# Kernel tuning notes

Measured on AMD Instinct MI355X. Metric: run time of the kernel, lower is better.

## Reference

```python
import jax, jax.numpy as jnp
import numpy as np

N, M, D, O = 16384, 4096, 256, 256

def setup_inputs() -> dict:
    key = jax.random.key(0)
    k1, k2, k3, k4, k5, k6, k7 = jax.random.split(key, 7)
    H_fine = jax.random.normal(k1, (N, D), dtype=jnp.float32)
    H_coarse = jax.random.normal(k2, (M, D), dtype=jnp.float32)
    inter_channel_adj = jax.random.randint(k3, (N, M), 0, 2).astype(jnp.float32)
    # attention = nn.Linear(2D, 1): weight vector [2D], bias scalar
    wa = jax.random.normal(k4, (2 * D,), dtype=jnp.float32) * (1.0 / np.sqrt(2 * D))
    ba = jax.random.normal(k5, (1,), dtype=jnp.float32) * 0.01
    # transform = nn.Linear(D, O), xavier_uniform weight
    lim = np.sqrt(6.0 / (D + O)).astype(np.float32)
    Wt = jax.random.uniform(k6, (O, D), minval=-lim, maxval=lim, dtype=jnp.float32)
    bt = jax.random.normal(k7, (O,), dtype=jnp.float32) * 0.01
    return {"H_fine": H_fine, "H_coarse": H_coarse,
            "inter_channel_adj": inter_channel_adj,
            "wa": wa, "ba": ba, "Wt": Wt, "bt": bt}

def reference(H_fine, H_coarse, inter_channel_adj, wa, ba, Wt, bt):
    d = H_fine.shape[-1]
    # additive attention: score_ij = [hf_i ; hc_j] . wa + b
    # = hf_i . wa[:d] + hc_j . wa[d:] + b  (avoids [N,M,2D] concat)
    sf = H_fine @ wa[:d]            # [N]
    sc = H_coarse @ wa[d:]          # [M]
    scores = sf[:, None] + sc[None, :] + ba[0]        # [N, M]
    masked = scores * inter_channel_adj               # [N, M]
    weights = jax.nn.softmax(masked, axis=-1)         # [N, M]
    attn_out = weights @ H_coarse                     # [N, D]
    attn_out = attn_out + H_fine                      # add_self=True
    out = attn_out @ Wt.T + bt                        # [N, O]
    return jax.nn.relu(out)
```

## Files before the change

### kernel.cpp

```cpp
#include <hip/hip_runtime.h>
#include <hip/hip_bf16.h>
#include <stdint.h>

#define N_ 16384
#define M_ 4096
#define D_ 256
#define O_ 256

#define WS_T    0
#define WS_U    (64*1024)
#define WS_R    (80*1024)
#define WS_WTP  (96*1024)
#define WS_BP   (256*1024)

typedef float  f32x4  __attribute__((ext_vector_type(4)));
typedef short  short8 __attribute__((ext_vector_type(8)));

__device__ __forceinline__ unsigned short f2bf(float f) {
  uint32_t u = __float_as_uint(f);
  u += 0x7FFFu + ((u >> 16) & 1u);
  return (unsigned short)(u >> 16);
}
__device__ __forceinline__ uint32_t pack2bf(float a, float b) {
  return (uint32_t)f2bf(a) | ((uint32_t)f2bf(b) << 16);
}

__device__ __forceinline__ void gload_lds16(const void* g, void* l) {
  __builtin_amdgcn_global_load_lds(
      (const __attribute__((address_space(1))) void*)g,
      (__attribute__((address_space(3))) void*)l, 16, 0, 0);
}

__global__ __launch_bounds__(256) void rowdot_exp_kernel(
    const float* __restrict__ X, const float* __restrict__ w,
    const float* __restrict__ bias, float* __restrict__ outv) {
  int wv = threadIdx.x >> 6, lane = threadIdx.x & 63;
  int row = blockIdx.x * 4 + wv;
  const float4* x4 = (const float4*)(X + (size_t)row * D_);
  const float4* w4 = (const float4*)w;
  float4 xa = x4[lane], wa4 = w4[lane];
  float s = xa.x * wa4.x + xa.y * wa4.y + xa.z * wa4.z + xa.w * wa4.w;
#pragma unroll
  for (int off = 32; off > 0; off >>= 1) s += __shfl_xor(s, off);
  if (lane == 0) outv[row] = expf(s + (bias ? bias[0] : 0.0f));
}

__global__ __launch_bounds__(256) void hc_pack_kernel(
    const float* __restrict__ Hc, unsigned short* __restrict__ BP,
    float* __restrict__ R) {
  __shared__ float tile[64][65];
  __shared__ float red[4][64];
  int bk = blockIdx.x >> 2;
  int bc = blockIdx.x & 3;
  int k0 = bk * 64, col0 = bc * 64;
  int t = threadIdx.x;
  int lane = t & 63, wv = t >> 6;
  int m = lane & 15, q = lane >> 4;
  float colsum = 0.0f;
#pragma unroll
  for (int i = 0; i < 16; ++i) {
    int e = t + 256 * i;
    int kk = e >> 6, cc = e & 63;
    float v = Hc[(size_t)(k0 + kk) * D_ + col0 + cc];
    tile[kk][cc] = v;
    colsum += v;
  }
  red[wv][t & 63] = colsum;
  __syncthreads();
  if (t < 64)
    atomicAdd(&R[col0 + t], red[0][t] + red[1][t] + red[2][t] + red[3][t]);
#pragma unroll
  for (int t8 = 0; t8 < 2; ++t8) {
    int tile_id = t8 * 4 + wv;
    int sub = tile_id >> 2, g = tile_id & 3;
    int kgg = bk * 2 + sub;
    int cgg = bc * 4 + g;
    short8 v8;
#pragma unroll
    for (int j = 0; j < 8; ++j)
      v8[j] = (short)f2bf(tile[sub * 32 + q * 8 + j][g * 16 + m]);
    *(short8*)(BP + ((size_t)(kgg * 16 + cgg) * 64 + lane) * 8) = v8;
  }
}

__global__ __launch_bounds__(256) void wt_pack_kernel(
    const float* __restrict__ Wt, unsigned short* __restrict__ WtP) {
  int t = blockIdx.x * 256 + threadIdx.x;
  int lane = t & 63, cg = (t >> 6) & 15, kg = t >> 10;
  int m = lane & 15, q = lane >> 4;
  const float* src = Wt + (size_t)(cg * 16 + m) * D_ + kg * 32 + q * 8;
  float4 w0 = *(const float4*)src, w1 = *(const float4*)(src + 4);
  short8 v8;
  v8[0] = (short)f2bf(w0.x); v8[1] = (short)f2bf(w0.y);
  v8[2] = (short)f2bf(w0.z); v8[3] = (short)f2bf(w0.w);
  v8[4] = (short)f2bf(w1.x); v8[5] = (short)f2bf(w1.y);
  v8[6] = (short)f2bf(w1.z); v8[7] = (short)f2bf(w1.w);
  *(short8*)(WtP + (size_t)t * 8) = v8;
}

__global__ __launch_bounds__(512, 4) void main_fused_kernel(
    const float* __restrict__ adj, const unsigned short* __restrict__ BP,
    const float* __restrict__ tv, const float* __restrict__ uv,
    const float* __restrict__ Rv, const float* __restrict__ Hf,
    const unsigned short* __restrict__ WtP, const float* __restrict__ bt,
    float* __restrict__ out) {
  union SM {
    struct {
      unsigned short B[2][16][512];
      unsigned int   A[2][2][256];
    } st;
    unsigned short attn[32][264];
  };
  __shared__ SM sm;
  __shared__ float Lrow[32];

  int tid = threadIdx.x;
  int w = tid >> 6, lane = tid & 63;
  int rtile = w & 1, cq = w >> 1;
  int q = lane >> 4, m = lane & 15;
  int i0 = blockIdx.x * 32;

  int srow = tid >> 4;
  int kin  = (tid & 15) * 2;
  int rts  = srow >> 4;
  int sdw  = (((kin >> 3) * 16 + (srow & 15)) << 2) + ((kin & 7) >> 1);
  const float* adjp = adj + (size_t)(i0 + srow) * M_ + kin;
  const float* up   = uv + kin;
  float t_reg = tv[i0 + srow];

  f32x4 acc[4];
#pragma unroll
  for (int n = 0; n < 4; ++n) acc[n] = (f32x4){0.f, 0.f, 0.f, 0.f};
  float rs = 0.0f;

#pragma unroll
  for (int c = 0; c < 2; ++c) {
    int cg = w * 2 + c;
    gload_lds16(BP + ((size_t)cg * 64 + lane) * 8, &sm.st.B[0][cg][0]);
  }
  {
    float2 a0 = *(const float2*)adjp;
    float2 uu = *(const float2*)up;
    float p0 = fmaf(a0.x, t_reg * uu.x, -a0.x);
    float p1 = fmaf(a0.y, t_reg * uu.y, -a0.y);
    rs += p0 + p1;
    sm.st.A[0][rts][sdw] = pack2bf(p0, p1);
  }
  float2 aA = *(const float2*)(adjp + 32);
  float2 aB = *(const float2*)(adjp + 64);
  __syncthreads();

  for (int kc = 0; kc < 128; ++kc) {
    int buf = kc & 1, nbuf = buf ^ 1;
    if (kc < 127) {
#pragma unroll
      for (int c = 0; c < 2; ++c) {
        int cg = w * 2 + c;
        gload_lds16(BP + ((size_t)((kc + 1) * 16 + cg) * 64 + lane) * 8,
                    &sm.st.B[nbuf][cg][0]);
      }
    }
    int k3 = (kc + 3 < 128) ? (kc + 3) * 32 : 0;
    float2 aC = *(const float2*)(adjp + k3);

    short8 af = *(const short8*)((const unsigned short*)&sm.st.A[buf][rtile][0] +
                                 (size_t)lane * 8);
#pragma unroll
    for (int n = 0; n < 4; ++n) {
      short8 bf = *(const short8*)&sm.st.B[buf][cq * 4 + n][lane * 8];
      acc[n] = __builtin_amdgcn_mfma_f32_16x16x32_bf16(af, bf, acc[n], 0, 0, 0);
    }

    if (kc < 127) {
      float2 uu = *(const float2*)(up + (kc + 1) * 32);
      float p0 = fmaf(aA.x, t_reg * uu.x, -aA.x);
      float p1 = fmaf(aA.y, t_reg * uu.y, -aA.y);
      rs += p0 + p1;
      sm.st.A[nbuf][rts][sdw] = pack2bf(p0, p1);
    }
    aA = aB; aB = aC;
    __syncthreads();
  }

  rs += __shfl_xor(rs, 1);
  rs += __shfl_xor(rs, 2);
  rs += __shfl_xor(rs, 4);
  rs += __shfl_xor(rs, 8);
  if ((lane & 15) == 0) Lrow[w * 4 + (lane >> 4)] = rs;
  __syncthreads();

  float invL[4];
#pragma unroll
  for (int r = 0; r < 4; ++r)
    invL[r] = 1.0f / (Lrow[rtile * 16 + q * 4 + r] + (float)M_);

#pragma unroll
  for (int n = 0; n < 4; ++n) {
    int col = cq * 64 + n * 16 + m;
    float Rc = Rv[col];
#pragma unroll
    for (int r = 0; r < 4; ++r) {
      int rloc = rtile * 16 + q * 4 + r;
      size_t row = (size_t)i0 + rloc;
      float v = (acc[n][r] + Rc) * invL[r] + Hf[row * D_ + col];
      sm.attn[rloc][col] = f2bf(v);
    }
  }
  __syncthreads();

  f32x4 facc[4];
#pragma unroll
  for (int n = 0; n < 4; ++n) facc[n] = (f32x4){0.f, 0.f, 0.f, 0.f};
  const unsigned short* wwave = WtP + (size_t)(cq * 4) * 512 + (size_t)lane * 8;
#pragma unroll
  for (int kf = 0; kf < 8; ++kf) {
    short8 af = *(const short8*)&sm.attn[rtile * 16 + m][kf * 32 + q * 8];
#pragma unroll
    for (int n = 0; n < 4; ++n) {
      short8 bf = *(const short8*)(wwave + ((size_t)kf * 16 + n) * 512);
      facc[n] = __builtin_amdgcn_mfma_f32_16x16x32_bf16(af, bf, facc[n], 0, 0, 0);
    }
  }
#pragma unroll
  for (int n = 0; n < 4; ++n) {
    int col = cq * 64 + n * 16 + m;
    float b = bt[col];
#pragma unroll
    for (int r = 0; r < 4; ++r) {
      size_t row = (size_t)i0 + rtile * 16 + q * 4 + r;
      out[row * O_ + col] = fmaxf(facc[n][r] + b, 0.0f);
    }
  }
}

extern "C" void kernel_launch(void* const* d_in, const int* in_sizes, int n_in,
                              void* d_out, int out_size, void* d_ws, size_t ws_size,
                              hipStream_t stream) {
  const float* Hf  = (const float*)d_in[0];
  const float* Hc  = (const float*)d_in[1];
  const float* adj = (const float*)d_in[2];
  const float* wa  = (const float*)d_in[3];
  const float* ba  = (const float*)d_in[4];
  const float* Wt  = (const float*)d_in[5];
  const float* bt  = (const float*)d_in[6];
  float* out = (float*)d_out;

  char* ws = (char*)d_ws;
  float* tv = (float*)(ws + WS_T);
  float* uv = (float*)(ws + WS_U);
  float* Rv = (float*)(ws + WS_R);
  unsigned short* WtP = (unsigned short*)(ws + WS_WTP);
  unsigned short* BP  = (unsigned short*)(ws + WS_BP);

  hipMemsetAsync(Rv, 0, D_ * sizeof(float), stream);

  rowdot_exp_kernel<<<N_ / 4, 256, 0, stream>>>(Hf, wa, ba, tv);
  rowdot_exp_kernel<<<M_ / 4, 256, 0, stream>>>(Hc, wa + D_, nullptr, uv);
  hc_pack_kernel<<<256, 256, 0, stream>>>(Hc, BP, Rv);
  wt_pack_kernel<<<32, 256, 0, stream>>>(Wt, WtP);

  main_fused_kernel<<<N_ / 32, 512, 0, stream>>>(adj, BP, tv, uv, Rv, Hf, WtP, bt, out);
}
```

Before: 537.2 us.

## Split attention matmul over K halves with atomic reduction and separate epilogue

Replaces the single fused kernel with a split-K kernel: each of two blocks per 32-row tile handles half of the coarse dimension. The kernel reads adj and packed H_coarse straight into registers instead of staging through LDS with per-step barriers, and accumulates partial results and row sums into global buffers with atomics. A separate epilogue kernel then normalizes, adds H_fine and runs the output projection. The aim is more parallelism and removal of barrier stalls in the bandwidth-bound adj stream, at the cost of an extra 16 MB memset, atomic traffic and one more launch.

```diff
diff --git a/kernel.cpp b/kernel.cpp
--- a/kernel.cpp
+++ b/kernel.cpp
@@ -7,11 +7,13 @@
 #define D_ 256
 #define O_ 256
 
-#define WS_T    0
-#define WS_U    (64*1024)
-#define WS_R    (80*1024)
-#define WS_WTP  (96*1024)
-#define WS_BP   (256*1024)
+#define WS_T     0
+#define WS_U     65536
+#define WS_R     81920
+#define WS_LSUM  98304
+#define WS_WTP   163840
+#define WS_BP    294912
+#define WS_C     4194304
 
 typedef float  f32x4  __attribute__((ext_vector_type(4)));
 typedef short  short8 __attribute__((ext_vector_type(8)));
@@ -20,15 +22,6 @@
   uint32_t u = __float_as_uint(f);
   u += 0x7FFFu + ((u >> 16) & 1u);
   return (unsigned short)(u >> 16);
-}
-__device__ __forceinline__ uint32_t pack2bf(float a, float b) {
-  return (uint32_t)f2bf(a) | ((uint32_t)f2bf(b) << 16);
-}
-
-__device__ __forceinline__ void gload_lds16(const void* g, void* l) {
-  __builtin_amdgcn_global_load_lds(
-      (const __attribute__((address_space(1))) void*)g,
-      (__attribute__((address_space(3))) void*)l, 16, 0, 0);
 }
 
 __global__ __launch_bounds__(256) void rowdot_exp_kernel(
@@ -98,132 +91,161 @@
   *(short8*)(WtP + (size_t)t * 8) = v8;
 }
 
-__global__ __launch_bounds__(512, 4) void main_fused_kernel(
+__global__ __launch_bounds__(256, 4) void main_split_kernel(
     const float* __restrict__ adj, const unsigned short* __restrict__ BP,
     const float* __restrict__ tv, const float* __restrict__ uv,
+    float* __restrict__ Cbuf, float* __restrict__ Lsum) {
+  __shared__ float u_lds[2048];
+  int tid = threadIdx.x;
+  int w = tid >> 6, lane = tid & 63;
+  int q = lane >> 4, m = lane & 15;
+  int kh = blockIdx.x & 1, rb = blockIdx.x >> 1;
+  int i0 = rb * 32;
+  int c0 = w * 64;
+
+  for (int i = tid; i < 2048; i += 256) u_lds[i] = uv[kh * 2048 + i];
+
+  float t0 = tv[i0 + m], t1 = tv[i0 + 16 + m];
+  const float* ar0 = adj + (size_t)(i0 + m) * M_ + kh * 2048 + q * 8;
+  const float* ar1 = ar0 + (size_t)16 * M_;
+  const unsigned short* bb = BP + (size_t)(kh * 64 * 16 + w * 4) * 512 + (size_t)lane * 8;
+
+  f32x4 acc[2][4];
+#pragma unroll
+  for (int r = 0; r < 2; ++r)
+#pragma unroll
+    for (int n = 0; n < 4; ++n) acc[r][n] = (f32x4){0.f, 0.f, 0.f, 0.f};
+  float rs0 = 0.0f, rs1 = 0.0f;
+
+  __syncthreads();
+
+  float4 aX00 = *(const float4*)ar0, aX01 = *(const float4*)(ar0 + 4);
+  float4 aX10 = *(const float4*)ar1, aX11 = *(const float4*)(ar1 + 4);
+  short8 bX[4], bY[4];
+#pragma unroll
+  for (int n = 0; n < 4; ++n) bX[n] = *(const short8*)(bb + n * 512);
+  float4 aY00, aY01, aY10, aY11;
+
+#define XF(A0, A1, TR, U0, U1, RS, AF)                                  \
+  {                                                                     \
+    float ax[8] = {A0.x, A0.y, A0.z, A0.w, A1.x, A1.y, A1.z, A1.w};     \
+    float ux[8] = {U0.x, U0.y, U0.z, U0.w, U1.x, U1.y, U1.z, U1.w};     \
+    _Pragma("unroll") for (int j = 0; j < 8; ++j) {                     \
+      float p = fmaf(ax[j], TR * ux[j], -ax[j]);                        \
+      RS += p;                                                          \
+      AF[j] = (short)f2bf(p);                                           \
+    }                                                                   \
+  }
+
+  for (int kk = 0; kk < 64; kk += 2) {
+    {
+      const float* p0 = ar0 + (kk + 1) * 32;
+      const float* p1 = ar1 + (kk + 1) * 32;
+      aY00 = *(const float4*)p0; aY01 = *(const float4*)(p0 + 4);
+      aY10 = *(const float4*)p1; aY11 = *(const float4*)(p1 + 4);
+      const unsigned short* bp = bb + (size_t)(kk + 1) * 8192;
+#pragma unroll
+      for (int n = 0; n < 4; ++n) bY[n] = *(const short8*)(bp + n * 512);
+    }
+    {
+      float4 u0 = *(const float4*)&u_lds[kk * 32 + q * 8];
+      float4 u1 = *(const float4*)&u_lds[kk * 32 + q * 8 + 4];
+      short8 af0, af1;
+      XF(aX00, aX01, t0, u0, u1, rs0, af0);
+      XF(aX10, aX11, t1, u0, u1, rs1, af1);
+#pragma unroll
+      for (int n = 0; n < 4; ++n) {
+        acc[0][n] = __builtin_amdgcn_mfma_f32_16x16x32_bf16(af0, bX[n], acc[0][n], 0, 0, 0);
+        acc[1][n] = __builtin_amdgcn_mfma_f32_16x16x32_bf16(af1, bX[n], acc[1][n], 0, 0, 0);
+      }
+    }
+    {
+      int k2 = (kk + 2) & 63;
+      const float* p0 = ar0 + k2 * 32;
+      const float* p1 = ar1 + k2 * 32;
+      aX00 = *(const float4*)p0; aX01 = *(const float4*)(p0 + 4);
+      aX10 = *(const float4*)p1; aX11 = *(const float4*)(p1 + 4);
+      const unsigned short* bp = bb + (size_t)k2 * 8192;
+#pragma unroll
+      for (int n = 0; n < 4; ++n) bX[n] = *(const short8*)(bp + n * 512);
+    }
+    {
+      float4 u0 = *(const float4*)&u_lds[(kk + 1) * 32 + q * 8];
+      float4 u1 = *(const float4*)&u_lds[(kk + 1) * 32 + q * 8 + 4];
+      short8 af0, af1;
+      XF(aY00, aY01, t0, u0, u1, rs0, af0);
+      XF(aY10, aY11, t1, u0, u1, rs1, af1);
+#pragma unroll
+      for (int n = 0; n < 4; ++n) {
+        acc[0][n] = __builtin_amdgcn_mfma_f32_16x16x32_bf16(af0, bY[n], acc[0][n], 0, 0, 0);
+        acc[1][n] = __builtin_amdgcn_mfma_f32_16x16x32_bf16(af1, bY[n], acc[1][n], 0, 0, 0);
+      }
+    }
+  }
+#undef XF
+
+  rs0 += __shfl_xor(rs0, 16); rs0 += __shfl_xor(rs0, 32);
+  rs1 += __shfl_xor(rs1, 16); rs1 += __shfl_xor(rs1, 32);
+  if (w == 0 && lane < 16) {
+    atomicAdd(&Lsum[i0 + m], rs0);
+    atomicAdd(&Lsum[i0 + 16 + m], rs1);
+  }
+
+#pragma unroll
+  for (int r = 0; r < 2; ++r)
+#pragma unroll
+    for (int n = 0; n < 4; ++n) {
+      int col = c0 + n * 16 + m;
+#pragma unroll
+      for (int j = 0; j < 4; ++j) {
+        int row = i0 + r * 16 + q * 4 + j;
+        atomicAdd(&Cbuf[(size_t)row * D_ + col], acc[r][n][j]);
+      }
+    }
+}
+
+__global__ __launch_bounds__(256, 4) void epilogue_kernel(
+    const float* __restrict__ Cbuf, const float* __restrict__ Lsum,
     const float* __restrict__ Rv, const float* __restrict__ Hf,
     const unsigned short* __restrict__ WtP, const float* __restrict__ bt,
     float* __restrict__ out) {
-  union SM {
-    struct {
-      unsigned short B[2][16][512];
-      unsigned int   A[2][2][256];
-    } st;
-    unsigned short attn[32][264];
-  };
-  __shared__ SM sm;
-  __shared__ float Lrow[32];
-
+  __shared__ alignas(16) unsigned short attn[32][264];
   int tid = threadIdx.x;
   int w = tid >> 6, lane = tid & 63;
-  int rtile = w & 1, cq = w >> 1;
+  int rtile = w & 1, chalf = w >> 1;
   int q = lane >> 4, m = lane & 15;
   int i0 = blockIdx.x * 32;
 
-  int srow = tid >> 4;
-  int kin  = (tid & 15) * 2;
-  int rts  = srow >> 4;
-  int sdw  = (((kin >> 3) * 16 + (srow & 15)) << 2) + ((kin & 7) >> 1);
-  const float* adjp = adj + (size_t)(i0 + srow) * M_ + kin;
-  const float* up   = uv + kin;
-  float t_reg = tv[i0 + srow];
-
-  f32x4 acc[4];
-#pragma unroll
-  for (int n = 0; n < 4; ++n) acc[n] = (f32x4){0.f, 0.f, 0.f, 0.f};
-  float rs = 0.0f;
-
-#pragma unroll
-  for (int c = 0; c < 2; ++c) {
-    int cg = w * 2 + c;
-    gload_lds16(BP + ((size_t)cg * 64 + lane) * 8, &sm.st.B[0][cg][0]);
-  }
-  {
-    float2 a0 = *(const float2*)adjp;
-    float2 uu = *(const float2*)up;
-    float p0 = fmaf(a0.x, t_reg * uu.x, -a0.x);
-    float p1 = fmaf(a0.y, t_reg * uu.y, -a0.y);
-    rs += p0 + p1;
-    sm.st.A[0][rts][sdw] = pack2bf(p0, p1);
-  }
-  float2 aA = *(const float2*)(adjp + 32);
-  float2 aB = *(const float2*)(adjp + 64);
+  float4 rv = *(const float4*)(Rv + lane * 4);
+#pragma unroll
+  for (int rr = 0; rr < 8; ++rr) {
+    int r = w * 8 + rr;
+    float invL = 1.0f / (Lsum[i0 + r] + (float)M_);
+    float4 cv = *(const float4*)(Cbuf + (size_t)(i0 + r) * D_ + lane * 4);
+    float4 hv = *(const float4*)(Hf + (size_t)(i0 + r) * D_ + lane * 4);
+    attn[r][lane * 4 + 0] = f2bf(fmaf(cv.x + rv.x, invL, hv.x));
+    attn[r][lane * 4 + 1] = f2bf(fmaf(cv.y + rv.y, invL, hv.y));
+    attn[r][lane * 4 + 2] = f2bf(fmaf(cv.z + rv.z, invL, hv.z));
+    attn[r][lane * 4 + 3] = f2bf(fmaf(cv.w + rv.w, invL, hv.w));
+  }
   __syncthreads();
 
-  for (int kc = 0; kc < 128; ++kc) {
-    int buf = kc & 1, nbuf = buf ^ 1;
-    if (kc < 127) {
-#pragma unroll
-      for (int c = 0; c < 2; ++c) {
-        int cg = w * 2 + c;
-        gload_lds16(BP + ((size_t)((kc + 1) * 16 + cg) * 64 + lane) * 8,
-                    &sm.st.B[nbuf][cg][0]);
-      }
-    }
-    int k3 = (kc + 3 < 128) ? (kc + 3) * 32 : 0;
-    float2 aC = *(const float2*)(adjp + k3);
-
-    short8 af = *(const short8*)((const unsigned short*)&sm.st.A[buf][rtile][0] +
-                                 (size_t)lane * 8);
-#pragma unroll
-    for (int n = 0; n < 4; ++n) {
-      short8 bf = *(const short8*)&sm.st.B[buf][cq * 4 + n][lane * 8];
-      acc[n] = __builtin_amdgcn_mfma_f32_16x16x32_bf16(af, bf, acc[n], 0, 0, 0);
-    }
-
-    if (kc < 127) {
-      float2 uu = *(const float2*)(up + (kc + 1) * 32);
-      float p0 = fmaf(aA.x, t_reg * uu.x, -aA.x);
-      float p1 = fmaf(aA.y, t_reg * uu.y, -aA.y);
-      rs += p0 + p1;
-      sm.st.A[nbuf][rts][sdw] = pack2bf(p0, p1);
-    }
-    aA = aB; aB = aC;
-    __syncthreads();
-  }
-
-  rs += __shfl_xor(rs, 1);
-  rs += __shfl_xor(rs, 2);
-  rs += __shfl_xor(rs, 4);
-  rs += __shfl_xor(rs, 8);
-  if ((lane & 15) == 0) Lrow[w * 4 + (lane >> 4)] = rs;
-  __syncthreads();
-
-  float invL[4];
-#pragma unroll
-  for (int r = 0; r < 4; ++r)
-    invL[r] = 1.0f / (Lrow[rtile * 16 + q * 4 + r] + (float)M_);
-
-#pragma unroll
-  for (int n = 0; n < 4; ++n) {
-    int col = cq * 64 + n * 16 + m;
-    float Rc = Rv[col];
-#pragma unroll
-    for (int r = 0; r < 4; ++r) {
-      int rloc = rtile * 16 + q * 4 + r;
-      size_t row = (size_t)i0 + rloc;
-      float v = (acc[n][r] + Rc) * invL[r] + Hf[row * D_ + col];
-      sm.attn[rloc][col] = f2bf(v);
-    }
-  }
-  __syncthreads();
-
-  f32x4 facc[4];
-#pragma unroll
-  for (int n = 0; n < 4; ++n) facc[n] = (f32x4){0.f, 0.f, 0.f, 0.f};
-  const unsigned short* wwave = WtP + (size_t)(cq * 4) * 512 + (size_t)lane * 8;
+  f32x4 facc[8];
+#pragma unroll
+  for (int n = 0; n < 8; ++n) facc[n] = (f32x4){0.f, 0.f, 0.f, 0.f};
+  const unsigned short* wwave = WtP + (size_t)chalf * 4096 + (size_t)lane * 8;
 #pragma unroll
   for (int kf = 0; kf < 8; ++kf) {
-    short8 af = *(const short8*)&sm.attn[rtile * 16 + m][kf * 32 + q * 8];
-#pragma unroll
-    for (int n = 0; n < 4; ++n) {
+    short8 af = *(const short8*)&attn[rtile * 16 + m][kf * 32 + q * 8];
+#pragma unroll
+    for (int n = 0; n < 8; ++n) {
       short8 bf = *(const short8*)(wwave + ((size_t)kf * 16 + n) * 512);
       facc[n] = __builtin_amdgcn_mfma_f32_16x16x32_bf16(af, bf, facc[n], 0, 0, 0);
     }
   }
 #pragma unroll
-  for (int n = 0; n < 4; ++n) {
-    int col = cq * 64 + n * 16 + m;
+  for (int n = 0; n < 8; ++n) {
+    int col = chalf * 128 + n * 16 + m;
     float b = bt[col];
 #pragma unroll
     for (int r = 0; r < 4; ++r) {
@@ -246,18 +268,23 @@
   float* out = (float*)d_out;
 
   char* ws = (char*)d_ws;
-  float* tv = (float*)(ws + WS_T);
-  float* uv = (float*)(ws + WS_U);
-  float* Rv = (float*)(ws + WS_R);
+  float* tv   = (float*)(ws + WS_T);
+  float* uv   = (float*)(ws + WS_U);
+  float* Rv   = (float*)(ws + WS_R);
+  float* Lsum = (float*)(ws + WS_LSUM);
   unsigned short* WtP = (unsigned short*)(ws + WS_WTP);
   unsigned short* BP  = (unsigned short*)(ws + WS_BP);
+  float* Cbuf = (float*)(ws + WS_C);
 
   hipMemsetAsync(Rv, 0, D_ * sizeof(float), stream);
+  hipMemsetAsync(Lsum, 0, N_ * sizeof(float), stream);
+  hipMemsetAsync(Cbuf, 0, (size_t)N_ * D_ * sizeof(float), stream);
 
   rowdot_exp_kernel<<<N_ / 4, 256, 0, stream>>>(Hf, wa, ba, tv);
   rowdot_exp_kernel<<<M_ / 4, 256, 0, stream>>>(Hc, wa + D_, nullptr, uv);
   hc_pack_kernel<<<256, 256, 0, stream>>>(Hc, BP, Rv);
   wt_pack_kernel<<<32, 256, 0, stream>>>(Wt, WtP);
 
-  main_fused_kernel<<<N_ / 32, 512, 0, stream>>>(adj, BP, tv, uv, Rv, Hf, WtP, bt, out);
-}
+  main_split_kernel<<<N_ / 32 * 2, 256, 0, stream>>>(adj, BP, tv, uv, Cbuf, Lsum);
+  epilogue_kernel<<<N_ / 32, 256, 0, stream>>>(Cbuf, Lsum, Rv, Hf, WtP, bt, out);
+}
```

Result: slower. 612.7 us (+14.1%).

## Split K across waves in main kernel and reduce partial accumulators via LDS atomics

Applied to the files above, without the earlier changes.

The main kernel is restructured so each of the 8 waves handles a disjoint 512-column K slice of the adjacency for all 32 rows and all 256 output columns. B fragments are read straight from global/L2 instead of being staged through LDS with barriers, and u is cached in LDS. Partial results are combined with LDS atomicAdds before the epilogue. This removes the per-step __syncthreads and LDS staging of the old pipelined loop. In exchange it needs 128 accumulator registers per lane, drops occupancy to 2 blocks per CU, and adds many LDS atomics. The workspace offset for BP also moves.

```diff
diff --git a/kernel.cpp b/kernel.cpp
--- a/kernel.cpp
+++ b/kernel.cpp
@@ -8,10 +8,10 @@
 #define O_ 256
 
 #define WS_T    0
-#define WS_U    (64*1024)
-#define WS_R    (80*1024)
-#define WS_WTP  (96*1024)
-#define WS_BP   (256*1024)
+#define WS_U    65536
+#define WS_R    81920
+#define WS_WTP  98304
+#define WS_BP   229376
 
 typedef float  f32x4  __attribute__((ext_vector_type(4)));
 typedef short  short8 __attribute__((ext_vector_type(8)));
@@ -21,14 +21,11 @@
   u += 0x7FFFu + ((u >> 16) & 1u);
   return (unsigned short)(u >> 16);
 }
-__device__ __forceinline__ uint32_t pack2bf(float a, float b) {
-  return (uint32_t)f2bf(a) | ((uint32_t)f2bf(b) << 16);
-}
-
-__device__ __forceinline__ void gload_lds16(const void* g, void* l) {
-  __builtin_amdgcn_global_load_lds(
-      (const __attribute__((address_space(1))) void*)g,
-      (__attribute__((address_space(3))) void*)l, 16, 0, 0);
+__device__ __forceinline__ uint32_t cvtpk(float a, float b) {
+  __hip_bfloat162 h = __float22bfloat162_rn(float2{a, b});
+  uint32_t u;
+  __builtin_memcpy(&u, &h, 4);
+  return u;
 }
 
 __global__ __launch_bounds__(256) void rowdot_exp_kernel(
@@ -98,132 +95,150 @@
   *(short8*)(WtP + (size_t)t * 8) = v8;
 }
 
-__global__ __launch_bounds__(512, 4) void main_fused_kernel(
+__device__ __forceinline__ short8 transform8(float4 A0, float4 A1, float t,
+                                             float4 u0, float4 u1, float& rs) {
+  float p0 = fmaf(A0.x, t * u0.x, -A0.x);
+  float p1 = fmaf(A0.y, t * u0.y, -A0.y);
+  float p2 = fmaf(A0.z, t * u0.z, -A0.z);
+  float p3 = fmaf(A0.w, t * u0.w, -A0.w);
+  float p4 = fmaf(A1.x, t * u1.x, -A1.x);
+  float p5 = fmaf(A1.y, t * u1.y, -A1.y);
+  float p6 = fmaf(A1.z, t * u1.z, -A1.z);
+  float p7 = fmaf(A1.w, t * u1.w, -A1.w);
+  rs += ((p0 + p1) + (p2 + p3)) + ((p4 + p5) + (p6 + p7));
+  union { short8 s; uint32_t u[4]; } r;
+  r.u[0] = cvtpk(p0, p1);
+  r.u[1] = cvtpk(p2, p3);
+  r.u[2] = cvtpk(p4, p5);
+  r.u[3] = cvtpk(p6, p7);
+  return r.s;
+}
+
+__global__ __launch_bounds__(512, 2) void mega_kernel(
     const float* __restrict__ adj, const unsigned short* __restrict__ BP,
     const float* __restrict__ tv, const float* __restrict__ uv,
     const float* __restrict__ Rv, const float* __restrict__ Hf,
     const unsigned short* __restrict__ WtP, const float* __restrict__ bt,
     float* __restrict__ out) {
-  union SM {
-    struct {
-      unsigned short B[2][16][512];
-      unsigned int   A[2][2][256];
-    } st;
-    unsigned short attn[32][264];
-  };
-  __shared__ SM sm;
+  __shared__ float u_lds[M_];
+  __shared__ float part[32][260];
+  __shared__ float redd[8][32];
   __shared__ float Lrow[32];
+  __shared__ alignas(16) unsigned short attn[32][264];
 
   int tid = threadIdx.x;
   int w = tid >> 6, lane = tid & 63;
-  int rtile = w & 1, cq = w >> 1;
   int q = lane >> 4, m = lane & 15;
   int i0 = blockIdx.x * 32;
 
-  int srow = tid >> 4;
-  int kin  = (tid & 15) * 2;
-  int rts  = srow >> 4;
-  int sdw  = (((kin >> 3) * 16 + (srow & 15)) << 2) + ((kin & 7) >> 1);
-  const float* adjp = adj + (size_t)(i0 + srow) * M_ + kin;
-  const float* up   = uv + kin;
-  float t_reg = tv[i0 + srow];
-
-  f32x4 acc[4];
-#pragma unroll
-  for (int n = 0; n < 4; ++n) acc[n] = (f32x4){0.f, 0.f, 0.f, 0.f};
-  float rs = 0.0f;
-
-#pragma unroll
-  for (int c = 0; c < 2; ++c) {
-    int cg = w * 2 + c;
-    gload_lds16(BP + ((size_t)cg * 64 + lane) * 8, &sm.st.B[0][cg][0]);
-  }
+  for (int i = tid; i < M_; i += 512) u_lds[i] = uv[i];
   {
-    float2 a0 = *(const float2*)adjp;
-    float2 uu = *(const float2*)up;
-    float p0 = fmaf(a0.x, t_reg * uu.x, -a0.x);
-    float p1 = fmaf(a0.y, t_reg * uu.y, -a0.y);
-    rs += p0 + p1;
-    sm.st.A[0][rts][sdw] = pack2bf(p0, p1);
-  }
-  float2 aA = *(const float2*)(adjp + 32);
-  float2 aB = *(const float2*)(adjp + 64);
-  __syncthreads();
-
-  for (int kc = 0; kc < 128; ++kc) {
-    int buf = kc & 1, nbuf = buf ^ 1;
-    if (kc < 127) {
-#pragma unroll
-      for (int c = 0; c < 2; ++c) {
-        int cg = w * 2 + c;
-        gload_lds16(BP + ((size_t)((kc + 1) * 16 + cg) * 64 + lane) * 8,
-                    &sm.st.B[nbuf][cg][0]);
-      }
-    }
-    int k3 = (kc + 3 < 128) ? (kc + 3) * 32 : 0;
-    float2 aC = *(const float2*)(adjp + k3);
-
-    short8 af = *(const short8*)((const unsigned short*)&sm.st.A[buf][rtile][0] +
-                                 (size_t)lane * 8);
+    float* pz = &part[0][0];
+    for (int i = tid; i < 32 * 260; i += 512) pz[i] = 0.0f;
+  }
+
+  float t0 = tv[i0 + m], t1 = tv[i0 + 16 + m];
+  const float* a0 = adj + (size_t)(i0 + m) * M_ + w * 512 + q * 8;
+  const float* a1 = a0 + (size_t)16 * M_;
+
+  f32x4 acc[2][16];
+#pragma unroll
+  for (int s = 0; s < 2; ++s)
+#pragma unroll
+    for (int n = 0; n < 16; ++n) acc[s][n] = (f32x4){0.f, 0.f, 0.f, 0.f};
+  float rs0 = 0.0f, rs1 = 0.0f;
+
+  __syncthreads();
+
+  float4 pa0 = *(const float4*)(a0);
+  float4 pa1 = *(const float4*)(a0 + 4);
+  float4 pb0 = *(const float4*)(a1);
+  float4 pb1 = *(const float4*)(a1 + 4);
+
+  for (int i = 0; i < 16; ++i) {
+    int inx = (i + 1 < 16) ? i + 1 : 0;
+    float4 na0 = *(const float4*)(a0 + inx * 32);
+    float4 na1 = *(const float4*)(a0 + inx * 32 + 4);
+    float4 nb0 = *(const float4*)(a1 + inx * 32);
+    float4 nb1 = *(const float4*)(a1 + inx * 32 + 4);
+
+    int kg = w * 16 + i;
+    float4 u0 = *(const float4*)&u_lds[kg * 32 + q * 8];
+    float4 u1 = *(const float4*)&u_lds[kg * 32 + q * 8 + 4];
+    short8 af0 = transform8(pa0, pa1, t0, u0, u1, rs0);
+    short8 af1 = transform8(pb0, pb1, t1, u0, u1, rs1);
+
+    const unsigned short* bk = BP + (size_t)(kg * 16) * 512 + (size_t)lane * 8;
+    short8 bcur = *(const short8*)(bk);
+#pragma unroll
+    for (int n = 0; n < 16; ++n) {
+      short8 bnext = bcur;
+      if (n < 15) bnext = *(const short8*)(bk + (size_t)(n + 1) * 512);
+      acc[0][n] = __builtin_amdgcn_mfma_f32_16x16x32_bf16(af0, bcur, acc[0][n], 0, 0, 0);
+      acc[1][n] = __builtin_amdgcn_mfma_f32_16x16x32_bf16(af1, bcur, acc[1][n], 0, 0, 0);
+      bcur = bnext;
+    }
+    pa0 = na0; pa1 = na1; pb0 = nb0; pb1 = nb1;
+  }
+
+  rs0 += __shfl_xor(rs0, 16); rs0 += __shfl_xor(rs0, 32);
+  rs1 += __shfl_xor(rs1, 16); rs1 += __shfl_xor(rs1, 32);
+  if (lane < 16) { redd[w][m] = rs0; redd[w][16 + m] = rs1; }
+
+#pragma unroll
+  for (int s = 0; s < 2; ++s)
+#pragma unroll
+    for (int n = 0; n < 16; ++n) {
+      int col = n * 16 + m;
+#pragma unroll
+      for (int r = 0; r < 4; ++r)
+        atomicAdd(&part[s * 16 + q * 4 + r][col], acc[s][n][r]);
+    }
+  __syncthreads();
+
+  if (tid < 32) {
+    float S = 0.0f;
+#pragma unroll
+    for (int ww = 0; ww < 8; ++ww) S += redd[ww][tid];
+    Lrow[tid] = S;
+  }
+  __syncthreads();
+
+#pragma unroll
+  for (int rr = 0; rr < 4; ++rr) {
+    int r = w * 4 + rr;
+    float invL = 1.0f / (Lrow[r] + (float)M_);
+    size_t grow = (size_t)(i0 + r) * D_;
+#pragma unroll
+    for (int h = 0; h < 2; ++h) {
+      int c = h * 128 + 2 * lane;
+      float2 pv = *(const float2*)&part[r][c];
+      float2 rv = *(const float2*)(Rv + c);
+      float2 hv = *(const float2*)(Hf + grow + c);
+      float v0 = fmaf(pv.x + rv.x, invL, hv.x);
+      float v1 = fmaf(pv.y + rv.y, invL, hv.y);
+      *(uint32_t*)&attn[r][c] = cvtpk(v0, v1);
+    }
+  }
+  __syncthreads();
+
+  int rtile = w & 1, c64 = w >> 1;
+  f32x4 facc[4];
+#pragma unroll
+  for (int n = 0; n < 4; ++n) facc[n] = (f32x4){0.f, 0.f, 0.f, 0.f};
+#pragma unroll
+  for (int kf = 0; kf < 8; ++kf) {
+    short8 af = *(const short8*)&attn[rtile * 16 + m][kf * 32 + q * 8];
 #pragma unroll
     for (int n = 0; n < 4; ++n) {
-      short8 bf = *(const short8*)&sm.st.B[buf][cq * 4 + n][lane * 8];
-      acc[n] = __builtin_amdgcn_mfma_f32_16x16x32_bf16(af, bf, acc[n], 0, 0, 0);
-    }
-
-    if (kc < 127) {
-      float2 uu = *(const float2*)(up + (kc + 1) * 32);
-      float p0 = fmaf(aA.x, t_reg * uu.x, -aA.x);
-      float p1 = fmaf(aA.y, t_reg * uu.y, -aA.y);
-      rs += p0 + p1;
-      sm.st.A[nbuf][rts][sdw] = pack2bf(p0, p1);
-    }
-    aA = aB; aB = aC;
-    __syncthreads();
-  }
-
-  rs += __shfl_xor(rs, 1);
-  rs += __shfl_xor(rs, 2);
-  rs += __shfl_xor(rs, 4);
-  rs += __shfl_xor(rs, 8);
-  if ((lane & 15) == 0) Lrow[w * 4 + (lane >> 4)] = rs;
-  __syncthreads();
-
-  float invL[4];
-#pragma unroll
-  for (int r = 0; r < 4; ++r)
-    invL[r] = 1.0f / (Lrow[rtile * 16 + q * 4 + r] + (float)M_);
-
+      int cg = c64 * 4 + n;
+      short8 bf = *(const short8*)(WtP + ((size_t)(kf * 16 + cg) * 64 + lane) * 8);
+      facc[n] = __builtin_amdgcn_mfma_f32_16x16x32_bf16(af, bf, facc[n], 0, 0, 0);
+    }
+  }
 #pragma unroll
   for (int n = 0; n < 4; ++n) {
-    int col = cq * 64 + n * 16 + m;
-    float Rc = Rv[col];
-#pragma unroll
-    for (int r = 0; r < 4; ++r) {
-      int rloc = rtile * 16 + q * 4 + r;
-      size_t row = (size_t)i0 + rloc;
-      float v = (acc[n][r] + Rc) * invL[r] + Hf[row * D_ + col];
-      sm.attn[rloc][col] = f2bf(v);
-    }
-  }
-  __syncthreads();
-
-  f32x4 facc[4];
-#pragma unroll
-  for (int n = 0; n < 4; ++n) facc[n] = (f32x4){0.f, 0.f, 0.f, 0.f};
-  const unsigned short* wwave = WtP + (size_t)(cq * 4) * 512 + (size_t)lane * 8;
-#pragma unroll
-  for (int kf = 0; kf < 8; ++kf) {
-    short8 af = *(const short8*)&sm.attn[rtile * 16 + m][kf * 32 + q * 8];
-#pragma unroll
-    for (int n = 0; n < 4; ++n) {
-      short8 bf = *(const short8*)(wwave + ((size_t)kf * 16 + n) * 512);
-      facc[n] = __builtin_amdgcn_mfma_f32_16x16x32_bf16(af, bf, facc[n], 0, 0, 0);
-    }
-  }
-#pragma unroll
-  for (int n = 0; n < 4; ++n) {
-    int col = cq * 64 + n * 16 + m;
+    int col = c64 * 64 + n * 16 + m;
     float b = bt[col];
 #pragma unroll
     for (int r = 0; r < 4; ++r) {
@@ -259,5 +274,5 @@
   hc_pack_kernel<<<256, 256, 0, stream>>>(Hc, BP, Rv);
   wt_pack_kernel<<<32, 256, 0, stream>>>(Wt, WtP);
 
-  main_fused_kernel<<<N_ / 32, 512, 0, stream>>>(adj, BP, tv, uv, Rv, Hf, WtP, bt, out);
-}
+  mega_kernel<<<N_ / 32, 512, 0, stream>>>(adj, BP, tv, uv, Rv, Hf, WtP, bt, out);
+}
```

Result: slower. 618.2 us (+15.1%).
